# Kernel tuning notes

Hardware: AMD Instinct MI355X
Metric: run time of the kernel (lower is better)

Reference implementation:

```python
import jax, jax.numpy as jnp
import numpy as np

N_NODES = 100000
N_EDGES = 1600000
IN_FT = 128
OUT_FT = 128


def setup_inputs() -> dict:
    key = jax.random.key(0)
    k1, k2, k3, k4, k5, k6 = jax.random.split(key, 6)
    stdv = 1.0 / np.sqrt(OUT_FT)
    x = jax.random.normal(k1, (N_NODES, IN_FT), dtype=jnp.float32)
    edge_rows = jax.random.randint(k2, (N_EDGES,), 0, N_NODES, dtype=jnp.int32)
    edge_cols = jax.random.randint(k3, (N_EDGES,), 0, N_NODES, dtype=jnp.int32)
    # normalized adjacency values (positive, like D^-1 A)
    edge_vals = jax.random.uniform(k4, (N_EDGES,), dtype=jnp.float32)
    W = jax.random.uniform(k5, (IN_FT, OUT_FT), dtype=jnp.float32, minval=-stdv, maxval=stdv)
    b = jax.random.uniform(k6, (OUT_FT,), dtype=jnp.float32, minval=-stdv, maxval=stdv)
    return {"x": x, "edge_rows": edge_rows, "edge_cols": edge_cols,
            "edge_vals": edge_vals, "W": W, "b": b}


def reference(x, edge_rows, edge_cols, edge_vals, W, b):
    # dense projection + bias: [N, out_ft]
    h = x @ W + b
    # SpMM: out[r] = sum_e vals[e] * h[cols[e]] for edges with rows[e] == r
    msgs = edge_vals[:, None] * h[edge_cols]          # [E, out_ft]
    out = jax.ops.segment_sum(msgs, edge_rows, num_segments=N_NODES)
    return jax.nn.relu(out)
```

## Files before the change

kernel.cpp:

```cpp
#include <hip/hip_runtime.h>

#define N_NODES 100000
#define N_EDGES 1600000
#define FT 128

#define NBUCK 391
#define EPB 4096
#define NBLKP ((N_EDGES + EPB - 1) / EPB)
#define CAP 1536
#define GEMM_BLOCKS ((N_NODES + 255) / 256)
#define SPMM_GRID (8 * 4 * ((NBUCK + 7) / 8))

#define OFF_H 0
#define OFF_BUCKETED 25600000
#define OFF_BLKHIST 38400000
#define OFF_BTOT 39011524
#define OFF_BBASE 39013088
#define WS_NEEDED 39014656

typedef __attribute__((ext_vector_type(8))) short bf16x8;
typedef __attribute__((ext_vector_type(4))) float f32x4;

static __device__ __forceinline__ ushort f2bf(float f) {
  const unsigned u = __float_as_uint(f);
  return (ushort)((u + 0x7FFF + ((u >> 16) & 1)) >> 16);
}
static __device__ __forceinline__ float bf2f(ushort s) {
  return __uint_as_float((unsigned)s << 16);
}

__global__ __launch_bounds__(256) void partA_kernel(
    const int* __restrict__ erows, int* __restrict__ blkhist) {
  __shared__ int cnt[NBUCK];
  const int tid = threadIdx.x;
  for (int j = tid; j < NBUCK; j += 256) cnt[j] = 0;
  __syncthreads();

  const int base4 = blockIdx.x * (EPB / 4);
#pragma unroll
  for (int it = 0; it < EPB / 4 / 256; ++it) {
    const int idx4 = base4 + it * 256 + tid;
    if (idx4 < N_EDGES / 4) {
      const int4 r = ((const int4*)erows)[idx4];
      atomicAdd(&cnt[r.x >> 8], 1);
      atomicAdd(&cnt[r.y >> 8], 1);
      atomicAdd(&cnt[r.z >> 8], 1);
      atomicAdd(&cnt[r.w >> 8], 1);
    }
  }
  __syncthreads();
  int* dst = blkhist + (size_t)blockIdx.x * NBUCK;
  for (int j = tid; j < NBUCK; j += 256) dst[j] = cnt[j];
}

__global__ __launch_bounds__(512) void partB1_kernel(
    int* __restrict__ blkhist, int* __restrict__ btot) {
  __shared__ int ps[512];
  const int b = blockIdx.x;
  const int t = threadIdx.x;
  int v = 0;
  if (t < NBLKP) v = blkhist[(size_t)t * NBUCK + b];
  ps[t] = v;
  __syncthreads();
#pragma unroll
  for (int d = 1; d < 512; d <<= 1) {
    const int u = (t >= d) ? ps[t - d] : 0;
    __syncthreads();
    ps[t] += u;
    __syncthreads();
  }
  if (t < NBLKP) blkhist[(size_t)t * NBUCK + b] = ps[t] - v;
  if (t == NBLKP - 1) btot[b] = ps[t];
}

__global__ __launch_bounds__(512) void partB2_kernel(
    const int* __restrict__ btot, int* __restrict__ bucket_base) {
  __shared__ int ps[512];
  const int t = threadIdx.x;
  int v = (t < NBUCK) ? btot[t] : 0;
  ps[t] = v;
  __syncthreads();
#pragma unroll
  for (int d = 1; d < 512; d <<= 1) {
    const int u = (t >= d) ? ps[t - d] : 0;
    __syncthreads();
    ps[t] += u;
    __syncthreads();
  }
  if (t < NBUCK) bucket_base[t] = ps[t] - v;
  if (t == NBUCK - 1) bucket_base[NBUCK] = N_EDGES;
}

__global__ __launch_bounds__(256) void fused_gemm_partC_kernel(
    const float* __restrict__ x,
    const float* __restrict__ W,
    const float* __restrict__ b,
    ushort* __restrict__ h,
    const int* __restrict__ erows,
    const int* __restrict__ ecols,
    const float* __restrict__ evals,
    const int* __restrict__ blkhist,
    const int* __restrict__ bucket_base,
    int2* __restrict__ bucketed) {
  __shared__ __align__(16) ushort whi[16384];
  __shared__ int cur[NBUCK];
  const int tid = threadIdx.x;

  if (blockIdx.x < GEMM_BLOCKS) {
    for (int idx = tid; idx < 16384; idx += 256) {
      const int k = idx >> 7;
      const int col = idx & 127;
      const ushort hi = f2bf(W[idx]);
      const int lane_ = (((k >> 3) & 3) << 4) | (col & 15);
      const int pos =
          ((((k >> 5) << 3) + (col >> 4)) * 64 + lane_) * 8 + (k & 7);
      whi[pos] = hi;
    }
    __syncthreads();

    const int w = tid >> 6;
    const int lane = tid & 63;
    const int r0 = blockIdx.x * 256 + w * 64;
    const int arow = lane & 15;
    const int kgrp = (lane >> 4) << 3;

    float bias_v[8];
#pragma unroll
    for (int ct = 0; ct < 8; ++ct) bias_v[ct] = b[ct * 16 + (lane & 15)];

    f32x4 acc[4][8];
#pragma unroll
    for (int rf = 0; rf < 4; ++rf)
#pragma unroll
      for (int ct = 0; ct < 8; ++ct) acc[rf][ct] = (f32x4){0.f, 0.f, 0.f, 0.f};

#pragma unroll
    for (int ks = 0; ks < 4; ++ks) {
      bf16x8 afr[4];
#pragma unroll
      for (int rf = 0; rf < 4; ++rf) {
        int r = r0 + rf * 16 + arow;
        r = (r < N_NODES) ? r : (N_NODES - 1);
        const float* xp = x + (size_t)r * FT + ks * 32 + kgrp;
        const float4 u0 = *(const float4*)xp;
        const float4 u1 = *(const float4*)(xp + 4);
        bf16x8 a;
        a[0] = (short)f2bf(u0.x);
        a[1] = (short)f2bf(u0.y);
        a[2] = (short)f2bf(u0.z);
        a[3] = (short)f2bf(u0.w);
        a[4] = (short)f2bf(u1.x);
        a[5] = (short)f2bf(u1.y);
        a[6] = (short)f2bf(u1.z);
        a[7] = (short)f2bf(u1.w);
        afr[rf] = a;
      }
#pragma unroll
      for (int ct = 0; ct < 8; ++ct) {
        const int fo = ((ks * 8 + ct) * 64 + lane) * 8;
        const bf16x8 bh = *(const bf16x8*)&whi[fo];
#pragma unroll
        for (int rf = 0; rf < 4; ++rf) {
          acc[rf][ct] = __builtin_amdgcn_mfma_f32_16x16x32_bf16(
              afr[rf], bh, acc[rf][ct], 0, 0, 0);
        }
      }
    }

    const int crow0 = (lane >> 4) << 2;
    const int ccol = lane & 15;
#pragma unroll
    for (int rf = 0; rf < 4; ++rf) {
#pragma unroll
      for (int ct = 0; ct < 8; ++ct) {
        const int col = ct * 16 + ccol;
#pragma unroll
        for (int i = 0; i < 4; ++i) {
          const int row = r0 + rf * 16 + crow0 + i;
          if (row < N_NODES)
            h[(size_t)row * FT + col] = f2bf(acc[rf][ct][i] + bias_v[ct]);
        }
      }
    }
  } else {
    const int bid = blockIdx.x - GEMM_BLOCKS;
    const int* src = blkhist + (size_t)bid * NBUCK;
    for (int j = tid; j < NBUCK; j += 256) cur[j] = src[j] + bucket_base[j];
    __syncthreads();

    const int base4 = bid * (EPB / 4);
#pragma unroll
    for (int it = 0; it < EPB / 4 / 256; ++it) {
      const int idx4 = base4 + it * 256 + tid;
      if (idx4 < N_EDGES / 4) {
        const int4 r = ((const int4*)erows)[idx4];
        const int4 c = ((const int4*)ecols)[idx4];
        const float4 v = ((const float4*)evals)[idx4];
        int p;
        p = atomicAdd(&cur[r.x >> 8], 1);
        bucketed[p] = (int2){((r.x & 255) << 24) | c.x, __float_as_int(v.x)};
        p = atomicAdd(&cur[r.y >> 8], 1);
        bucketed[p] = (int2){((r.y & 255) << 24) | c.y, __float_as_int(v.y)};
        p = atomicAdd(&cur[r.z >> 8], 1);
        bucketed[p] = (int2){((r.z & 255) << 24) | c.z, __float_as_int(v.z)};
        p = atomicAdd(&cur[r.w >> 8], 1);
        bucketed[p] = (int2){((r.w & 255) << 24) | c.w, __float_as_int(v.w)};
      }
    }
  }
}

__global__ __launch_bounds__(512) void spmm_bucket_kernel(
    const int2* __restrict__ bucketed,
    const int* __restrict__ bucket_base,
    const ushort* __restrict__ h,
    float* __restrict__ out) {
  __shared__ int2 tmp[CAP];
  __shared__ int2 eds[CAP];
  __shared__ int cnt[64];
  __shared__ int pos[64];
  __shared__ int cur[64];
  __shared__ int ns;
  const int p_ = blockIdx.x;
  const int x_ = p_ & 7;
  const int m_ = p_ >> 3;
  const int q = m_ & 3;
  const int b = 8 * (m_ >> 2) + x_;
  if (b >= NBUCK) return;
  const int t = threadIdx.x;
  const int beg = bucket_base[b];
  const int end = bucket_base[b + 1];

  if (t < 64) cnt[t] = 0;
  if (t == 0) ns = 0;
  __syncthreads();

  for (int i = beg + t; i < end; i += 512) {
    const int2 rec = bucketed[i];
    const int r8 = ((unsigned)rec.x) >> 24;
    if ((r8 >> 6) == q) {
      const int p = atomicAdd(&ns, 1);
      if (p < CAP) {
        tmp[p] = rec;
        atomicAdd(&cnt[r8 & 63], 1);
      }
    }
  }
  __syncthreads();

  const int m = (ns < CAP) ? ns : CAP;
  const bool overflow = (ns > CAP);

  if (t < 64) pos[t] = cnt[t];
  __syncthreads();
#pragma unroll
  for (int d = 1; d < 64; d <<= 1) {
    int u = 0;
    if (t < 64 && t >= d) u = pos[t - d];
    __syncthreads();
    if (t < 64) pos[t] += u;
    __syncthreads();
  }
  if (t < 64) {
    const int excl = pos[t] - cnt[t];
    pos[t] = excl;
    cur[t] = excl;
  }
  __syncthreads();

  for (int i = t; i < m; i += 512) {
    const int2 rec = tmp[i];
    const int r6 = (((unsigned)rec.x) >> 24) & 63;
    const int p = atomicAdd(&cur[r6], 1);
    eds[p] = (int2){rec.x & 0x00FFFFFF, rec.y};
  }
  __syncthreads();

  const int g = t >> 5;
  const int lane = t & 31;
  const int j = lane * 4;

  for (int rr = 0; rr < 4; ++rr) {
    const int r = rr * 16 + g;
    const int row = b * 256 + q * 64 + r;
    const int rbeg = pos[r];
    const int rend = cur[r];

    float a0 = 0.f, a1 = 0.f, a2 = 0.f, a3 = 0.f;
    int e = rbeg;
    for (; e + 3 < rend; e += 4) {
      const int2 p0 = eds[e];
      const int2 p1 = eds[e + 1];
      const int2 p2 = eds[e + 2];
      const int2 p3 = eds[e + 3];
      const ushort4 q0 = *(const ushort4*)(h + (size_t)p0.x * FT + j);
      const ushort4 q1 = *(const ushort4*)(h + (size_t)p1.x * FT + j);
      const ushort4 q2 = *(const ushort4*)(h + (size_t)p2.x * FT + j);
      const ushort4 q3 = *(const ushort4*)(h + (size_t)p3.x * FT + j);
      const float v0 = __int_as_float(p0.y);
      const float v1 = __int_as_float(p1.y);
      const float v2 = __int_as_float(p2.y);
      const float v3 = __int_as_float(p3.y);
      a0 = fmaf(v0, bf2f(q0.x), a0);
      a1 = fmaf(v0, bf2f(q0.y), a1);
      a2 = fmaf(v0, bf2f(q0.z), a2);
      a3 = fmaf(v0, bf2f(q0.w), a3);
      a0 = fmaf(v1, bf2f(q1.x), a0);
      a1 = fmaf(v1, bf2f(q1.y), a1);
      a2 = fmaf(v1, bf2f(q1.z), a2);
      a3 = fmaf(v1, bf2f(q1.w), a3);
      a0 = fmaf(v2, bf2f(q2.x), a0);
      a1 = fmaf(v2, bf2f(q2.y), a1);
      a2 = fmaf(v2, bf2f(q2.z), a2);
      a3 = fmaf(v2, bf2f(q2.w), a3);
      a0 = fmaf(v3, bf2f(q3.x), a0);
      a1 = fmaf(v3, bf2f(q3.y), a1);
      a2 = fmaf(v3, bf2f(q3.z), a2);
      a3 = fmaf(v3, bf2f(q3.w), a3);
    }
    for (; e < rend; ++e) {
      const int2 p0 = eds[e];
      const float v0 = __int_as_float(p0.y);
      const ushort4 q0 = *(const ushort4*)(h + (size_t)p0.x * FT + j);
      a0 = fmaf(v0, bf2f(q0.x), a0);
      a1 = fmaf(v0, bf2f(q0.y), a1);
      a2 = fmaf(v0, bf2f(q0.z), a2);
      a3 = fmaf(v0, bf2f(q0.w), a3);
    }
    if (overflow) {
      int seen = 0;
      const int have = rend - rbeg;
      for (int i = beg; i < end; ++i) {
        const int2 rec = bucketed[i];
        const int r8 = ((unsigned)rec.x) >> 24;
        if ((r8 >> 6) == q && (r8 & 63) == r) {
          ++seen;
          if (seen > have) {
            const float v0 = __int_as_float(rec.y);
            const ushort4 q0 =
                *(const ushort4*)(h + (size_t)(rec.x & 0x00FFFFFF) * FT + j);
            a0 = fmaf(v0, bf2f(q0.x), a0);
            a1 = fmaf(v0, bf2f(q0.y), a1);
            a2 = fmaf(v0, bf2f(q0.z), a2);
            a3 = fmaf(v0, bf2f(q0.w), a3);
          }
        }
      }
    }

    if (row < N_NODES) {
      float4 o;
      o.x = fmaxf(a0, 0.f);
      o.y = fmaxf(a1, 0.f);
      o.z = fmaxf(a2, 0.f);
      o.w = fmaxf(a3, 0.f);
      *(float4*)(out + (size_t)row * FT + j) = o;
    }
  }
}

__global__ __launch_bounds__(256) void gemm_bias_kernel(
    const float* __restrict__ x,
    const float* __restrict__ W,
    const float* __restrict__ b,
    ushort* __restrict__ h) {
  __shared__ __align__(16) ushort whi[16384];
  const int tid = threadIdx.x;

  for (int idx = tid; idx < 16384; idx += 256) {
    const int k = idx >> 7;
    const int col = idx & 127;
    const ushort hi = f2bf(W[idx]);
    const int lane_ = (((k >> 3) & 3) << 4) | (col & 15);
    const int pos = ((((k >> 5) << 3) + (col >> 4)) * 64 + lane_) * 8 + (k & 7);
    whi[pos] = hi;
  }
  __syncthreads();

  const int w = tid >> 6;
  const int lane = tid & 63;
  const int r0 = blockIdx.x * 256 + w * 64;
  const int arow = lane & 15;
  const int kgrp = (lane >> 4) << 3;

  float bias_v[8];
#pragma unroll
  for (int ct = 0; ct < 8; ++ct) bias_v[ct] = b[ct * 16 + (lane & 15)];

  f32x4 acc[4][8];
#pragma unroll
  for (int rf = 0; rf < 4; ++rf)
#pragma unroll
    for (int ct = 0; ct < 8; ++ct) acc[rf][ct] = (f32x4){0.f, 0.f, 0.f, 0.f};

#pragma unroll
  for (int ks = 0; ks < 4; ++ks) {
    bf16x8 afr[4];
#pragma unroll
    for (int rf = 0; rf < 4; ++rf) {
      int r = r0 + rf * 16 + arow;
      r = (r < N_NODES) ? r : (N_NODES - 1);
      const float* xp = x + (size_t)r * FT + ks * 32 + kgrp;
      const float4 u0 = *(const float4*)xp;
      const float4 u1 = *(const float4*)(xp + 4);
      bf16x8 a;
      a[0] = (short)f2bf(u0.x);
      a[1] = (short)f2bf(u0.y);
      a[2] = (short)f2bf(u0.z);
      a[3] = (short)f2bf(u0.w);
      a[4] = (short)f2bf(u1.x);
      a[5] = (short)f2bf(u1.y);
      a[6] = (short)f2bf(u1.z);
      a[7] = (short)f2bf(u1.w);
      afr[rf] = a;
    }
#pragma unroll
    for (int ct = 0; ct < 8; ++ct) {
      const int fo = ((ks * 8 + ct) * 64 + lane) * 8;
      const bf16x8 bh = *(const bf16x8*)&whi[fo];
#pragma unroll
      for (int rf = 0; rf < 4; ++rf) {
        acc[rf][ct] = __builtin_amdgcn_mfma_f32_16x16x32_bf16(
            afr[rf], bh, acc[rf][ct], 0, 0, 0);
      }
    }
  }

  const int crow0 = (lane >> 4) << 2;
  const int ccol = lane & 15;
#pragma unroll
  for (int rf = 0; rf < 4; ++rf) {
#pragma unroll
    for (int ct = 0; ct < 8; ++ct) {
      const int col = ct * 16 + ccol;
#pragma unroll
      for (int i = 0; i < 4; ++i) {
        const int row = r0 + rf * 16 + crow0 + i;
        if (row < N_NODES)
          h[(size_t)row * FT + col] = f2bf(acc[rf][ct][i] + bias_v[ct]);
      }
    }
  }
}

__global__ __launch_bounds__(256) void edge_scatter_kernel(
    const int* __restrict__ erows,
    const int* __restrict__ ecols,
    const float* __restrict__ evals,
    const ushort* __restrict__ h,
    float* out) {
  const int tid = threadIdx.x;
  const int e = blockIdx.x * 8 + (tid >> 5);
  if (e >= N_EDGES) return;
  const int r = erows[e];
  const int c = ecols[e];
  const float v = evals[e];
  const int j = (tid & 31) * 4;
  const ushort4 q = *(const ushort4*)(h + (size_t)c * FT + j);
  float* op = out + (size_t)r * FT + j;
  atomicAdd(op + 0, v * bf2f(q.x));
  atomicAdd(op + 1, v * bf2f(q.y));
  atomicAdd(op + 2, v * bf2f(q.z));
  atomicAdd(op + 3, v * bf2f(q.w));
}

__global__ __launch_bounds__(256) void relu_kernel(float* out, int n4) {
  const int i = blockIdx.x * blockDim.x + threadIdx.x;
  if (i < n4) {
    float4 v = ((float4*)out)[i];
    v.x = fmaxf(v.x, 0.f);
    v.y = fmaxf(v.y, 0.f);
    v.z = fmaxf(v.z, 0.f);
    v.w = fmaxf(v.w, 0.f);
    ((float4*)out)[i] = v;
  }
}

extern "C" void kernel_launch(void* const* d_in, const int* in_sizes, int n_in,
                              void* d_out, int out_size, void* d_ws, size_t ws_size,
                              hipStream_t stream) {
  const float* x = (const float*)d_in[0];
  const int* erows = (const int*)d_in[1];
  const int* ecols = (const int*)d_in[2];
  const float* evals = (const float*)d_in[3];
  const float* W = (const float*)d_in[4];
  const float* b = (const float*)d_in[5];
  float* out = (float*)d_out;

  char* ws = (char*)d_ws;
  ushort* h = (ushort*)(ws + OFF_H);

  if (ws_size >= (size_t)WS_NEEDED) {
    int2* bucketed = (int2*)(ws + OFF_BUCKETED);
    int* blkhist = (int*)(ws + OFF_BLKHIST);
    int* btot = (int*)(ws + OFF_BTOT);
    int* bucket_base = (int*)(ws + OFF_BBASE);

    partA_kernel<<<NBLKP, 256, 0, stream>>>(erows, blkhist);
    partB1_kernel<<<NBUCK, 512, 0, stream>>>(blkhist, btot);
    partB2_kernel<<<1, 512, 0, stream>>>(btot, bucket_base);
    fused_gemm_partC_kernel<<<GEMM_BLOCKS + NBLKP, 256, 0, stream>>>(
        x, W, b, h, erows, ecols, evals, blkhist, bucket_base, bucketed);
    spmm_bucket_kernel<<<SPMM_GRID, 512, 0, stream>>>(bucketed, bucket_base,
                                                      h, out);
  } else {
    gemm_bias_kernel<<<GEMM_BLOCKS, 256, 0, stream>>>(x, W, b, h);
    hipMemsetAsync(d_out, 0, (size_t)out_size * sizeof(float), stream);
    edge_scatter_kernel<<<(N_EDGES + 7) / 8, 256, 0, stream>>>(erows, ecols,
                                                               evals, h, out);
    const int n4 = out_size / 4;
    relu_kernel<<<(n4 + 255) / 256, 256, 0, stream>>>(out, n4);
  }
}
```

Before: 115.6 us.

## Replace histogram and scan partitioning with fixed-capacity buckets and overflow list

Drops the separate histogram kernel and the two prefix-scan kernels. Each edge block now counts its edges per bucket in shared memory and reserves space in a fixed-capacity slot per bucket with one global atomic per bucket. Edges that do not fit go to a global overflow list, which the SpMM kernel scans for its row. This removes three launches and their serial dependencies, at the cost of reading row indices twice in the fused kernel, a larger workspace, and a nondeterministic edge order within each bucket.

```diff
diff --git a/kernel.cpp b/kernel.cpp
--- a/kernel.cpp
+++ b/kernel.cpp
@@ -8,15 +8,18 @@
 #define EPB 4096
 #define NBLKP ((N_EDGES + EPB - 1) / EPB)
 #define CAP 1536
+#define CAPB 4800
+#define OVFCAP 65536
 #define GEMM_BLOCKS ((N_NODES + 255) / 256)
 #define SPMM_GRID (8 * 4 * ((NBUCK + 7) / 8))
 
 #define OFF_H 0
 #define OFF_BUCKETED 25600000
-#define OFF_BLKHIST 38400000
-#define OFF_BTOT 39011524
-#define OFF_BBASE 39013088
-#define WS_NEEDED 39014656
+#define OFF_GCUR 40614400
+#define OFF_NOVF 40615964
+#define OFF_OVFREC 40615968
+#define OFF_OVFBUCK 41140256
+#define WS_NEEDED 41402400
 
 typedef __attribute__((ext_vector_type(8))) short bf16x8;
 typedef __attribute__((ext_vector_type(4))) float f32x4;
@@ -27,68 +30,6 @@
 }
 static __device__ __forceinline__ float bf2f(ushort s) {
   return __uint_as_float((unsigned)s << 16);
-}
-
-__global__ __launch_bounds__(256) void partA_kernel(
-    const int* __restrict__ erows, int* __restrict__ blkhist) {
-  __shared__ int cnt[NBUCK];
-  const int tid = threadIdx.x;
-  for (int j = tid; j < NBUCK; j += 256) cnt[j] = 0;
-  __syncthreads();
-
-  const int base4 = blockIdx.x * (EPB / 4);
-#pragma unroll
-  for (int it = 0; it < EPB / 4 / 256; ++it) {
-    const int idx4 = base4 + it * 256 + tid;
-    if (idx4 < N_EDGES / 4) {
-      const int4 r = ((const int4*)erows)[idx4];
-      atomicAdd(&cnt[r.x >> 8], 1);
-      atomicAdd(&cnt[r.y >> 8], 1);
-      atomicAdd(&cnt[r.z >> 8], 1);
-      atomicAdd(&cnt[r.w >> 8], 1);
-    }
-  }
-  __syncthreads();
-  int* dst = blkhist + (size_t)blockIdx.x * NBUCK;
-  for (int j = tid; j < NBUCK; j += 256) dst[j] = cnt[j];
-}
-
-__global__ __launch_bounds__(512) void partB1_kernel(
-    int* __restrict__ blkhist, int* __restrict__ btot) {
-  __shared__ int ps[512];
-  const int b = blockIdx.x;
-  const int t = threadIdx.x;
-  int v = 0;
-  if (t < NBLKP) v = blkhist[(size_t)t * NBUCK + b];
-  ps[t] = v;
-  __syncthreads();
-#pragma unroll
-  for (int d = 1; d < 512; d <<= 1) {
-    const int u = (t >= d) ? ps[t - d] : 0;
-    __syncthreads();
-    ps[t] += u;
-    __syncthreads();
-  }
-  if (t < NBLKP) blkhist[(size_t)t * NBUCK + b] = ps[t] - v;
-  if (t == NBLKP - 1) btot[b] = ps[t];
-}
-
-__global__ __launch_bounds__(512) void partB2_kernel(
-    const int* __restrict__ btot, int* __restrict__ bucket_base) {
-  __shared__ int ps[512];
-  const int t = threadIdx.x;
-  int v = (t < NBUCK) ? btot[t] : 0;
-  ps[t] = v;
-  __syncthreads();
-#pragma unroll
-  for (int d = 1; d < 512; d <<= 1) {
-    const int u = (t >= d) ? ps[t - d] : 0;
-    __syncthreads();
-    ps[t] += u;
-    __syncthreads();
-  }
-  if (t < NBUCK) bucket_base[t] = ps[t] - v;
-  if (t == NBUCK - 1) bucket_base[NBUCK] = N_EDGES;
 }
 
 __global__ __launch_bounds__(256) void fused_gemm_partC_kernel(
@@ -99,11 +40,13 @@
     const int* __restrict__ erows,
     const int* __restrict__ ecols,
     const float* __restrict__ evals,
-    const int* __restrict__ blkhist,
-    const int* __restrict__ bucket_base,
+    int* gcur,
+    int* novf,
+    int2* __restrict__ ovf_rec,
+    int* __restrict__ ovf_buck,
     int2* __restrict__ bucketed) {
   __shared__ __align__(16) ushort whi[16384];
-  __shared__ int cur[NBUCK];
+  __shared__ int cnt[NBUCK];
   const int tid = threadIdx.x;
 
   if (blockIdx.x < GEMM_BLOCKS) {
@@ -184,11 +127,31 @@
     }
   } else {
     const int bid = blockIdx.x - GEMM_BLOCKS;
-    const int* src = blkhist + (size_t)bid * NBUCK;
-    for (int j = tid; j < NBUCK; j += 256) cur[j] = src[j] + bucket_base[j];
+    for (int j = tid; j < NBUCK; j += 256) cnt[j] = 0;
     __syncthreads();
 
     const int base4 = bid * (EPB / 4);
+#pragma unroll
+    for (int it = 0; it < EPB / 4 / 256; ++it) {
+      const int idx4 = base4 + it * 256 + tid;
+      if (idx4 < N_EDGES / 4) {
+        const int4 r = ((const int4*)erows)[idx4];
+        atomicAdd(&cnt[r.x >> 8], 1);
+        atomicAdd(&cnt[r.y >> 8], 1);
+        atomicAdd(&cnt[r.z >> 8], 1);
+        atomicAdd(&cnt[r.w >> 8], 1);
+      }
+    }
+    __syncthreads();
+
+    for (int j = tid; j < NBUCK; j += 256) {
+      const int hj = cnt[j];
+      int base = 0;
+      if (hj > 0) base = atomicAdd(&gcur[j], hj);
+      cnt[j] = j * CAPB + ((base < CAPB) ? base : CAPB);
+    }
+    __syncthreads();
+
 #pragma unroll
     for (int it = 0; it < EPB / 4 / 256; ++it) {
       const int idx4 = base4 + it * 256 + tid;
@@ -196,15 +159,25 @@
         const int4 r = ((const int4*)erows)[idx4];
         const int4 c = ((const int4*)ecols)[idx4];
         const float4 v = ((const float4*)evals)[idx4];
-        int p;
-        p = atomicAdd(&cur[r.x >> 8], 1);
-        bucketed[p] = (int2){((r.x & 255) << 24) | c.x, __float_as_int(v.x)};
-        p = atomicAdd(&cur[r.y >> 8], 1);
-        bucketed[p] = (int2){((r.y & 255) << 24) | c.y, __float_as_int(v.y)};
-        p = atomicAdd(&cur[r.z >> 8], 1);
-        bucketed[p] = (int2){((r.z & 255) << 24) | c.z, __float_as_int(v.z)};
-        p = atomicAdd(&cur[r.w >> 8], 1);
-        bucketed[p] = (int2){((r.w & 255) << 24) | c.w, __float_as_int(v.w)};
+        int bb, p, lim;
+        int2 rec;
+#define SCAT(RR, CC, VV)                                           \
+        bb = (RR) >> 8;                                            \
+        rec.x = (((RR) & 255) << 24) | (CC);                       \
+        rec.y = __float_as_int(VV);                                \
+        p = atomicAdd(&cnt[bb], 1);                                \
+        lim = bb * CAPB + CAPB;                                    \
+        if (p < lim) {                                             \
+          bucketed[p] = rec;                                       \
+        } else {                                                   \
+          const int op = atomicAdd(novf, 1);                       \
+          if (op < OVFCAP) { ovf_rec[op] = rec; ovf_buck[op] = bb; } \
+        }
+        SCAT(r.x, c.x, v.x)
+        SCAT(r.y, c.y, v.y)
+        SCAT(r.z, c.z, v.z)
+        SCAT(r.w, c.w, v.w)
+#undef SCAT
       }
     }
   }
@@ -212,7 +185,10 @@
 
 __global__ __launch_bounds__(512) void spmm_bucket_kernel(
     const int2* __restrict__ bucketed,
-    const int* __restrict__ bucket_base,
+    const int* __restrict__ gcur,
+    const int* __restrict__ novf,
+    const int2* __restrict__ ovf_rec,
+    const int* __restrict__ ovf_buck,
     const ushort* __restrict__ h,
     float* __restrict__ out) {
   __shared__ int2 tmp[CAP];
@@ -228,8 +204,10 @@
   const int b = 8 * (m_ >> 2) + x_;
   if (b >= NBUCK) return;
   const int t = threadIdx.x;
-  const int beg = bucket_base[b];
-  const int end = bucket_base[b + 1];
+  const int beg = b * CAPB;
+  const int fill = gcur[b];
+  const int end = beg + ((fill < CAPB) ? fill : CAPB);
+  const int nov = *novf;
 
   if (t < 64) cnt[t] = 0;
   if (t == 0) ns = 0;
@@ -347,6 +325,24 @@
         }
       }
     }
+    if (nov > 0) {
+      const int lim = (nov < OVFCAP) ? nov : OVFCAP;
+      for (int i = 0; i < lim; ++i) {
+        if (ovf_buck[i] == b) {
+          const int2 rec = ovf_rec[i];
+          const int r8 = ((unsigned)rec.x) >> 24;
+          if ((r8 >> 6) == q && (r8 & 63) == r) {
+            const float v0 = __int_as_float(rec.y);
+            const ushort4 q0 =
+                *(const ushort4*)(h + (size_t)(rec.x & 0x00FFFFFF) * FT + j);
+            a0 = fmaf(v0, bf2f(q0.x), a0);
+            a1 = fmaf(v0, bf2f(q0.y), a1);
+            a2 = fmaf(v0, bf2f(q0.z), a2);
+            a3 = fmaf(v0, bf2f(q0.w), a3);
+          }
+        }
+      }
+    }
 
     if (row < N_NODES) {
       float4 o;
@@ -492,17 +488,17 @@
 
   if (ws_size >= (size_t)WS_NEEDED) {
     int2* bucketed = (int2*)(ws + OFF_BUCKETED);
-    int* blkhist = (int*)(ws + OFF_BLKHIST);
-    int* btot = (int*)(ws + OFF_BTOT);
-    int* bucket_base = (int*)(ws + OFF_BBASE);
-
-    partA_kernel<<<NBLKP, 256, 0, stream>>>(erows, blkhist);
-    partB1_kernel<<<NBUCK, 512, 0, stream>>>(blkhist, btot);
-    partB2_kernel<<<1, 512, 0, stream>>>(btot, bucket_base);
+    int* gcur = (int*)(ws + OFF_GCUR);
+    int* novf = (int*)(ws + OFF_NOVF);
+    int2* ovf_rec = (int2*)(ws + OFF_OVFREC);
+    int* ovf_buck = (int*)(ws + OFF_OVFBUCK);
+
+    hipMemsetAsync(gcur, 0, (NBUCK + 1) * sizeof(int), stream);
     fused_gemm_partC_kernel<<<GEMM_BLOCKS + NBLKP, 256, 0, stream>>>(
-        x, W, b, h, erows, ecols, evals, blkhist, bucket_base, bucketed);
-    spmm_bucket_kernel<<<SPMM_GRID, 512, 0, stream>>>(bucketed, bucket_base,
-                                                      h, out);
+        x, W, b, h, erows, ecols, evals, gcur, novf, ovf_rec, ovf_buck,
+        bucketed);
+    spmm_bucket_kernel<<<SPMM_GRID, 512, 0, stream>>>(
+        bucketed, gcur, novf, ovf_rec, ovf_buck, h, out);
   } else {
     gemm_bias_kernel<<<GEMM_BLOCKS, 256, 0, stream>>>(x, W, b, h);
     hipMemsetAsync(d_out, 0, (size_t)out_size * sizeof(float), stream);
```

After: 107.2 us (median of 2 runs). -7.2%, faster.
